# Optimization experiments

Measured on AMD Instinct MI355X. Metric: run time of the kernel, lower is better.

## Reference

```python
import jax, jax.numpy as jnp
import numpy as np

N = 10000       # nodes
E = 200000      # node pairs (edges) in rel_dict
R = 400000      # relation instances
F_IN = 128
F_OUT = 64


def setup_inputs() -> dict:
    key = jax.random.key(0)
    ks = jax.random.split(key, 8)
    x = jax.random.normal(ks[0], (N, F_IN), dtype=jnp.float32)
    rel = jax.random.normal(ks[1], (R, F_IN), dtype=jnp.float32)
    adj = jax.random.uniform(ks[2], (N, N), dtype=jnp.float32)
    edge_pairs = jax.random.randint(ks[3], (E, 2), 0, N, dtype=jnp.int32)
    rel_seg = jax.random.randint(ks[4], (R,), 0, E, dtype=jnp.int32)
    # Conv1d(in, out, kernel_size=1, bias=False) == Linear: weight [out, in]
    W = jax.random.normal(ks[5], (F_OUT, F_IN), dtype=jnp.float32) * 0.1
    w_rel = jax.random.normal(ks[6], (F_IN,), dtype=jnp.float32) * 0.1
    bias = jnp.zeros((F_OUT,), dtype=jnp.float32)
    return {"x": x, "rel": rel, "adj": adj, "edge_pairs": edge_pairs,
            "rel_seg": rel_seg, "W": W, "w_rel": w_rel, "bias": bias}


def reference(x, rel, adj, edge_pairs, rel_seg, W, w_rel, bias):
    # node transform: [N, F_OUT]
    seq_fts = x @ W.T
    # per-relation scalar: [R]
    fts_rel = rel @ w_rel
    # segment-mean per edge (vectorized form of the rel_dict loop)
    sums = jax.ops.segment_sum(fts_rel, rel_seg, num_segments=E)
    cnts = jax.ops.segment_sum(jnp.ones_like(fts_rel), rel_seg, num_segments=E)
    edge_means = sums / jnp.maximum(cnts, 1.0)  # [E]
    # symmetric scatter into dense logits [N, N]
    e1, e2 = edge_pairs[:, 0], edge_pairs[:, 1]
    logits = jnp.zeros_like(adj)
    logits = logits.at[e1, e2].set(edge_means).at[e2, e1].set(edge_means)
    # masked-ish softmax over rows, then sparse-weighted aggregation
    coefs = jax.nn.softmax(jax.nn.sigmoid(logits) + adj, axis=1)  # [N, N]
    # dropout is a no-op in eval mode (training=False)
    ret = coefs @ seq_fts + bias  # [N, F_OUT]
    return jax.nn.elu(ret)        # concat=True
```

## Files before the change

### kernel.cpp

```cpp
#include <hip/hip_runtime.h>
#include <math.h>

#define NN   10000
#define EE   200000
#define RR   400000
#define FIN  128
#define FOUT 64

#define HASH_BITS 20
#define HSIZE (1u << HASH_BITS)
#define HMASK (HSIZE - 1u)
#define ROWCAP 256

#define NKB 314

typedef __bf16 bf16x8 __attribute__((ext_vector_type(8)));
typedef __bf16 bf16x4 __attribute__((ext_vector_type(4)));
typedef float  f32x4  __attribute__((ext_vector_type(4)));

#define O_SUMS   0
#define O_CNTS   (O_SUMS + EE)
#define O_ROWCNT (O_CNTS + EE)
#define O_HKEY   (O_ROWCNT + NN)
#define O_HPRIO  (O_HKEY + HSIZE)
#define O_SEQTP  (O_HPRIO + HSIZE)
#define SEQTP_WORDS (NKB * 5 * 512 / 2)
#define ZERO_WORDS (O_SEQTP + SEQTP_WORDS)
#define O_NUMP   ZERO_WORDS
#define O_SP     (O_NUMP + 8 * NN * FOUT)
#define O_PAIRS  (O_SP + 8 * NN)

__global__ __launch_bounds__(256) void k_zero(f32x4* __restrict__ p, int n4) {
    int gid = blockIdx.x * 256 + threadIdx.x;
    if (gid < n4) p[gid] = (f32x4){0.f, 0.f, 0.f, 0.f};
}

__global__ __launch_bounds__(256) void k_seqfts(const float* __restrict__ x,
                                                const float* __restrict__ W,
                                                __bf16* __restrict__ seqTp) {
    __shared__ float Wt[FIN][FOUT + 1];
    __shared__ float xs[FIN][16 + 1];
    int t = threadIdx.x;
    for (int e = t; e < FOUT * FIN; e += 256) {
        int c = e >> 7, k = e & 127;
        Wt[k][c] = W[e];
    }
    int row0 = blockIdx.x * 16;
    for (int e = t; e < 16 * FIN; e += 256) {
        int r = e >> 7, k = e & 127;
        int gr = row0 + r;
        xs[k][r] = (gr < NN) ? x[(size_t)gr * FIN + k] : 0.f;
    }
    __syncthreads();
    int col = t & 63;
    int rg  = t >> 6;
    float acc[4] = {0.f, 0.f, 0.f, 0.f};
    for (int k = 0; k < FIN; ++k) {
        float w = Wt[k][col];
        #pragma unroll
        for (int i = 0; i < 4; ++i) acc[i] += w * xs[k][rg * 4 + i];
    }
    #pragma unroll
    for (int i = 0; i < 4; ++i) {
        int gr = row0 + rg * 4 + i;
        int kb = gr >> 5, g = (gr >> 3) & 3, slot = gr & 7;
        seqTp[((size_t)kb * 5 + (col >> 4)) * 512 + ((col & 15) + g * 16) * 8 + slot]
            = (__bf16)acc[i];
        if (col < 16)
            seqTp[((size_t)kb * 5 + 4) * 512 + (col + g * 16) * 8 + slot] = (__bf16)1.0f;
    }
}

__device__ __forceinline__ unsigned hash_cell(unsigned cell) {
    return (cell * 2654435761u) >> (32 - HASH_BITS);
}
__device__ __forceinline__ void entry_ij(const int* ep, int e, int& i, int& j, int& k) {
    k = (e < EE) ? e : e - EE;
    int a = ep[2 * k], b = ep[2 * k + 1];
    if (e < EE) { i = a; j = b; } else { i = b; j = a; }
}

#define BM 64
#define BK 64
#define KSPLIT 8
#define NCHUNK 157
#define CPK 20
#define MAINB (NCHUNK * KSPLIT)
#define ILV   11
#define MRB   (ILV * MAINB)
#define SCATAB ((2 * EE + 255) / 256)
#define GRID_MR (MRB + SCATAB)
#define LDAP 72

__global__ __launch_bounds__(256) void k_mainrel(const float* __restrict__ adj,
                                                 const __bf16* __restrict__ seqTp,
                                                 const float* __restrict__ rel,
                                                 const float* __restrict__ wrel,
                                                 const int* __restrict__ rseg,
                                                 const int* __restrict__ ep,
                                                 float* __restrict__ sums,
                                                 float* __restrict__ cnts,
                                                 unsigned* __restrict__ hkey,
                                                 unsigned* __restrict__ hprio,
                                                 float* __restrict__ Nump,
                                                 float* __restrict__ Sp) {
    __shared__ __bf16 As[2][BM][LDAP];
    int t   = threadIdx.x;
    int bid = blockIdx.x;

    if (bid >= MRB) {
        int e = (bid - MRB) * 256 + t;
        if (e >= 2 * EE) return;
        int i, j, k;
        entry_ij(ep, e, i, j, k);
        unsigned cell = (unsigned)i * NN + (unsigned)j;
        unsigned keyv = cell + 1u;
        unsigned h = hash_cell(cell);
        while (true) {
            unsigned old = atomicCAS(&hkey[h], 0u, keyv);
            if (old == 0u || old == keyv) break;
            h = (h + 1u) & HMASK;
        }
        atomicMax(&hprio[h], (unsigned)(e + 1));
        return;
    }

    if (bid % ILV) {
        int relb = bid - bid / ILV - 1;
        int lane = t & 31;
        f32x4 w = *(const f32x4*)(wrel + lane * 4);
        #pragma unroll
        for (int it = 0; it < 4; ++it) {
            int row = relb * 32 + it * 8 + (t >> 5);
            if (row < RR) {
                f32x4 v = *(const f32x4*)(rel + (size_t)row * FIN + lane * 4);
                float s = v.x * w.x + v.y * w.y + v.z * w.z + v.w * w.w;
                #pragma unroll
                for (int off = 16; off >= 1; off >>= 1) s += __shfl_xor(s, off, 64);
                if (lane == 0) {
                    int seg = rseg[row];
                    atomicAdd(&sums[seg], s);
                    atomicAdd(&cnts[seg], 1.0f);
                }
            }
        }
        return;
    }

    int mi   = bid / ILV;
    int rowc = mi % NCHUNK;
    int ks   = mi / NCHUNK;
    int row0 = rowc * BM;
    int c0   = ks * CPK;
    int c1   = min(NCHUNK, c0 + CPK);
    int w  = t >> 6, l = t & 63;
    int lr = l & 15, lk = l >> 4;
    int sr = t >> 4;
    int sk = (t & 15) * 4;

    f32x4 acc[5];
    #pragma unroll
    for (int n = 0; n < 5; ++n) acc[n] = (f32x4){0.f, 0.f, 0.f, 0.f};

    f32x4 pvA[4], pvB[4];

#define LOADA(PV, CH)                                                          \
    {                                                                          \
        int k0_ = (CH) * BK;                                                   \
        _Pragma("unroll")                                                      \
        for (int e2 = 0; e2 < 4; ++e2) {                                       \
            int gr = row0 + sr + e2 * 16;                                      \
            int gk = k0_ + sk;                                                 \
            PV[e2] = (gr < NN && gk < NN)                                      \
                         ? *(const f32x4*)(adj + (size_t)gr * NN + gk)         \
                         : (f32x4){-1e9f, -1e9f, -1e9f, -1e9f};                \
        }                                                                      \
    }

#define BODY(PV, CH, P_)                                                       \
    {                                                                          \
        _Pragma("unroll")                                                      \
        for (int e2 = 0; e2 < 4; ++e2) {                                       \
            f32x4 v = PV[e2];                                                  \
            float e0 = exp2f(fmaf(v.x, 1.442695041f, 0.7213475204f));          \
            float e1 = exp2f(fmaf(v.y, 1.442695041f, 0.7213475204f));          \
            float e2f = exp2f(fmaf(v.z, 1.442695041f, 0.7213475204f));         \
            float e3 = exp2f(fmaf(v.w, 1.442695041f, 0.7213475204f));          \
            bf16x4 q = { (__bf16)e0, (__bf16)e1, (__bf16)e2f, (__bf16)e3 };    \
            *(bf16x4*)&As[P_][sr + e2 * 16][sk] = q;                           \
        }                                                                      \
        const __bf16* bp = seqTp + (size_t)(CH) * 2 * 5 * 512 + l * 8;         \
        bf16x8 b0 = *(const bf16x8*)(bp);                                      \
        bf16x8 b1 = *(const bf16x8*)(bp + 512);                                \
        bf16x8 b2 = *(const bf16x8*)(bp + 1024);                               \
        bf16x8 b3 = *(const bf16x8*)(bp + 1536);                               \
        bf16x8 b4 = *(const bf16x8*)(bp + 2048);                               \
        __syncthreads();                                                       \
        bf16x8 a0 = *(const bf16x8*)&As[P_][w * 16 + lr][lk * 8];              \
        acc[0] = __builtin_amdgcn_mfma_f32_16x16x32_bf16(a0, b0, acc[0], 0, 0, 0); \
        acc[1] = __builtin_amdgcn_mfma_f32_16x16x32_bf16(a0, b1, acc[1], 0, 0, 0); \
        acc[2] = __builtin_amdgcn_mfma_f32_16x16x32_bf16(a0, b2, acc[2], 0, 0, 0); \
        acc[3] = __builtin_amdgcn_mfma_f32_16x16x32_bf16(a0, b3, acc[3], 0, 0, 0); \
        acc[4] = __builtin_amdgcn_mfma_f32_16x16x32_bf16(a0, b4, acc[4], 0, 0, 0); \
        const __bf16* bq = bp + 2560;                                          \
        bf16x8 d0 = *(const bf16x8*)(bq);                                      \
        bf16x8 d1 = *(const bf16x8*)(bq + 512);                                \
        bf16x8 d2 = *(const bf16x8*)(bq + 1024);                               \
        bf16x8 d3 = *(const bf16x8*)(bq + 1536);                               \
        bf16x8 d4 = *(const bf16x8*)(bq + 2048);                               \
        bf16x8 a1 = *(const bf16x8*)&As[P_][w * 16 + lr][32 + lk * 8];         \
        acc[0] = __builtin_amdgcn_mfma_f32_16x16x32_bf16(a1, d0, acc[0], 0, 0, 0); \
        acc[1] = __builtin_amdgcn_mfma_f32_16x16x32_bf16(a1, d1, acc[1], 0, 0, 0); \
        acc[2] = __builtin_amdgcn_mfma_f32_16x16x32_bf16(a1, d2, acc[2], 0, 0, 0); \
        acc[3] = __builtin_amdgcn_mfma_f32_16x16x32_bf16(a1, d3, acc[3], 0, 0, 0); \
        acc[4] = __builtin_amdgcn_mfma_f32_16x16x32_bf16(a1, d4, acc[4], 0, 0, 0); \
    }

    LOADA(pvA, c0);
    int ch = c0, p = 0;
    while (true) {
        if (ch + 1 < c1) LOADA(pvB, ch + 1);
        BODY(pvA, ch, p);
        p ^= 1; ++ch;
        if (ch >= c1) break;
        if (ch + 1 < c1) LOADA(pvA, ch + 1);
        BODY(pvB, ch, p);
        p ^= 1; ++ch;
        if (ch >= c1) break;
    }
#undef LOADA
#undef BODY

    float* nout = Nump + (size_t)ks * NN * FOUT;
    #pragma unroll
    for (int n = 0; n < 4; ++n) {
        #pragma unroll
        for (int r = 0; r < 4; ++r) {
            int grow = row0 + w * 16 + lk * 4 + r;
            if (grow < NN)
                nout[(size_t)grow * FOUT + n * 16 + lr] = acc[n][r];
        }
    }
    if (lr == 0) {
        #pragma unroll
        for (int r = 0; r < 4; ++r) {
            int grow = row0 + w * 16 + lk * 4 + r;
            if (grow < NN) Sp[(size_t)ks * NN + grow] = acc[4][r];
        }
    }
}

__global__ __launch_bounds__(256) void k_scatB(const int* __restrict__ ep,
                                               const float* __restrict__ sums,
                                               const float* __restrict__ cnts,
                                               const unsigned* __restrict__ hkey,
                                               const unsigned* __restrict__ hprio,
                                               const float* __restrict__ adj,
                                               int* __restrict__ rowcnt,
                                               uint2* __restrict__ pairs) {
    int e = blockIdx.x * 256 + threadIdx.x;
    if (e >= 2 * EE) return;
    int i, j, k;
    entry_ij(ep, e, i, j, k);
    unsigned cell = (unsigned)i * NN + (unsigned)j;
    unsigned keyv = cell + 1u;
    unsigned h = hash_cell(cell);
    while (hkey[h] != keyv) h = (h + 1u) & HMASK;
    if (hprio[h] == (unsigned)(e + 1)) {
        float v   = sums[k] / fmaxf(cnts[k], 1.0f);
        float sg  = 1.f / (1.f + __expf(-v));
        float aij = adj[(size_t)i * NN + j];
        float dw  = __expf(aij + sg) - __expf(aij + 0.5f);
        if (dw != 0.f) {
            int pos = atomicAdd(&rowcnt[i], 1);
            if (pos < ROWCAP)
                pairs[(size_t)i * ROWCAP + pos] =
                    make_uint2((unsigned)j, __float_as_uint(dw));
        }
    }
}

__global__ __launch_bounds__(256) void k_rowupd(const float* __restrict__ Nump,
                                                const float* __restrict__ Sp,
                                                const int* __restrict__ rowcnt,
                                                const uint2* __restrict__ pairs,
                                                const __bf16* __restrict__ seqTp,
                                                const float* __restrict__ bias,
                                                float* __restrict__ out) {
    int t = threadIdx.x;
    int i = blockIdx.x * 4 + (t >> 6);
    if (i >= NN) return;
    int c = t & 63;
    float acc = 0.f, sb = 0.f;
    #pragma unroll
    for (int ks = 0; ks < 8; ++ks) {
        acc += Nump[(size_t)ks * NN * FOUT + (size_t)i * FOUT + c];
        sb  += Sp[(size_t)ks * NN + i];
    }
    int cnt = min(rowcnt[i], ROWCAP);
    float sdw = 0.f;
    const uint2* pr = pairs + (size_t)i * ROWCAP;
    for (int e = 0; e < cnt; ++e) {
        uint2 pk = pr[e];
        float d  = __uint_as_float(pk.y);
        unsigned j = pk.x;
        float sj = (float)seqTp[((size_t)(j >> 5) * 5 + (c >> 4)) * 512
                                + ((c & 15) + ((j >> 3) & 3) * 16) * 8 + (j & 7)];
        acc += d * sj;
        sdw += d;
    }
    float v = acc / (sb + sdw) + bias[c];
    out[(size_t)i * FOUT + c] = (v > 0.f) ? v : expm1f(v);
}

extern "C" void kernel_launch(void* const* d_in, const int* in_sizes, int n_in,
                              void* d_out, int out_size, void* d_ws, size_t ws_size,
                              hipStream_t stream) {
    const float* x    = (const float*)d_in[0];
    const float* rel  = (const float*)d_in[1];
    const float* adj  = (const float*)d_in[2];
    const int*   ep   = (const int*)d_in[3];
    const int*   rseg = (const int*)d_in[4];
    const float* W    = (const float*)d_in[5];
    const float* wrel = (const float*)d_in[6];
    const float* bias = (const float*)d_in[7];
    float* out = (float*)d_out;

    float* ws = (float*)d_ws;
    float*    sums   = ws + O_SUMS;
    float*    cnts   = ws + O_CNTS;
    int*      rowcnt = (int*)(ws + O_ROWCNT);
    unsigned* hkey   = (unsigned*)(ws + O_HKEY);
    unsigned* hprio  = (unsigned*)(ws + O_HPRIO);
    __bf16*   seqTp  = (__bf16*)(ws + O_SEQTP);
    float*    Nump   = ws + O_NUMP;
    float*    Sp     = ws + O_SP;
    uint2*    pairs  = (uint2*)(ws + O_PAIRS);

    int n4 = ZERO_WORDS / 4;
    k_zero<<<(n4 + 255) / 256, 256, 0, stream>>>((f32x4*)d_ws, n4);
    k_seqfts<<<NN / 16, 256, 0, stream>>>(x, W, seqTp);
    k_mainrel<<<GRID_MR, 256, 0, stream>>>(adj, seqTp, rel, wrel, rseg, ep,
                                           sums, cnts, hkey, hprio, Nump, Sp);
    k_scatB<<<(2 * EE + 255) / 256, 256, 0, stream>>>(ep, sums, cnts, hkey, hprio,
                                                      adj, rowcnt, pairs);
    k_rowupd<<<(NN + 3) / 4, 256, 0, stream>>>(Nump, Sp, rowcnt, pairs,
                                               seqTp, bias, out);
}
```

Before: 319.7 us.

## Precompute bf16 exp(adj) in a conversion pass and fuse scatter into GEMM

Adds a pass that reads adj once, writes exp(adj+0.5) as a padded bf16 matrix and accumulates row sums via atomics, alongside the relation reductions and hash insertion. The GEMM kernel then streams the bf16 matrix directly, dropping the ones-column MFMA for row sums, and the edge scatter kernel is interleaved into the same launch. This removes exp work and fp32 loads from the GEMM inner loop at the cost of an extra 200MB write and read of workspace.

```diff
diff --git a/kernel.cpp b/kernel.cpp
--- a/kernel.cpp
+++ b/kernel.cpp
@@ -6,6 +6,7 @@
 #define RR   400000
 #define FIN  128
 #define FOUT 64
+#define AJP  10048
 
 #define HASH_BITS 20
 #define HSIZE (1u << HASH_BITS)
@@ -13,6 +14,8 @@
 #define ROWCAP 256
 
 #define NKB 314
+#define L2E 1.442695041f
+#define CHALF 0.7213475204f
 
 typedef __bf16 bf16x8 __attribute__((ext_vector_type(8)));
 typedef __bf16 bf16x4 __attribute__((ext_vector_type(4)));
@@ -20,15 +23,16 @@
 
 #define O_SUMS   0
 #define O_CNTS   (O_SUMS + EE)
-#define O_ROWCNT (O_CNTS + EE)
+#define O_S      (O_CNTS + EE)
+#define O_ROWCNT (O_S + NN)
 #define O_HKEY   (O_ROWCNT + NN)
 #define O_HPRIO  (O_HKEY + HSIZE)
 #define O_SEQTP  (O_HPRIO + HSIZE)
 #define SEQTP_WORDS (NKB * 5 * 512 / 2)
 #define ZERO_WORDS (O_SEQTP + SEQTP_WORDS)
-#define O_NUMP   ZERO_WORDS
-#define O_SP     (O_NUMP + 8 * NN * FOUT)
-#define O_PAIRS  (O_SP + 8 * NN)
+#define O_ADJE   ZERO_WORDS
+#define O_NUMP   (O_ADJE + NN * AJP / 2)
+#define O_PAIRS  (O_NUMP + 8 * NN * FOUT)
 
 __global__ __launch_bounds__(256) void k_zero(f32x4* __restrict__ p, int n4) {
     int gid = blockIdx.x * 256 + threadIdx.x;
@@ -66,8 +70,6 @@
         int kb = gr >> 5, g = (gr >> 3) & 3, slot = gr & 7;
         seqTp[((size_t)kb * 5 + (col >> 4)) * 512 + ((col & 15) + g * 16) * 8 + slot]
             = (__bf16)acc[i];
-        if (col < 16)
-            seqTp[((size_t)kb * 5 + 4) * 512 + (col + g * 16) * 8 + slot] = (__bf16)1.0f;
     }
 }
 
@@ -80,36 +82,25 @@
     if (e < EE) { i = a; j = b; } else { i = b; j = a; }
 }
 
-#define BM 64
-#define BK 64
-#define KSPLIT 8
-#define NCHUNK 157
-#define CPK 20
-#define MAINB (NCHUNK * KSPLIT)
-#define ILV   11
-#define MRB   (ILV * MAINB)
-#define SCATAB ((2 * EE + 255) / 256)
-#define GRID_MR (MRB + SCATAB)
-#define LDAP 72
-
-__global__ __launch_bounds__(256) void k_mainrel(const float* __restrict__ adj,
-                                                 const __bf16* __restrict__ seqTp,
+#define CRB 16250
+#define HASHB2 1563
+#define GRID_CR (CRB + HASHB2)
+
+__global__ __launch_bounds__(256) void k_convrel(const float* __restrict__ adj,
                                                  const float* __restrict__ rel,
                                                  const float* __restrict__ wrel,
                                                  const int* __restrict__ rseg,
                                                  const int* __restrict__ ep,
+                                                 __bf16* __restrict__ adjE,
+                                                 float* __restrict__ S,
                                                  float* __restrict__ sums,
                                                  float* __restrict__ cnts,
                                                  unsigned* __restrict__ hkey,
-                                                 unsigned* __restrict__ hprio,
-                                                 float* __restrict__ Nump,
-                                                 float* __restrict__ Sp) {
-    __shared__ __bf16 As[2][BM][LDAP];
-    int t   = threadIdx.x;
-    int bid = blockIdx.x;
-
-    if (bid >= MRB) {
-        int e = (bid - MRB) * 256 + t;
+                                                 unsigned* __restrict__ hprio) {
+    int t = threadIdx.x, bid = blockIdx.x;
+
+    if (bid >= CRB) {
+        int e = (bid - CRB) * 256 + t;
         if (e >= 2 * EE) return;
         int i, j, k;
         entry_ij(ep, e, i, j, k);
@@ -125,95 +116,168 @@
         return;
     }
 
-    if (bid % ILV) {
-        int relb = bid - bid / ILV - 1;
-        int lane = t & 31;
-        f32x4 w = *(const f32x4*)(wrel + lane * 4);
+    int m = bid % 13;
+    int grp = bid / 13;
+    int l = t & 63;
+
+    if (m >= 8) {
+        int relb = grp * 5 + (m - 8);
+        int lane = l & 31;
+        f32x4 wv = *(const f32x4*)(wrel + lane * 4);
+        int rbase = relb * 64 + (t >> 5);
+        f32x4 pv[8];
         #pragma unroll
-        for (int it = 0; it < 4; ++it) {
-            int row = relb * 32 + it * 8 + (t >> 5);
-            if (row < RR) {
-                f32x4 v = *(const f32x4*)(rel + (size_t)row * FIN + lane * 4);
-                float s = v.x * w.x + v.y * w.y + v.z * w.z + v.w * w.w;
-                #pragma unroll
-                for (int off = 16; off >= 1; off >>= 1) s += __shfl_xor(s, off, 64);
-                if (lane == 0) {
-                    int seg = rseg[row];
-                    atomicAdd(&sums[seg], s);
-                    atomicAdd(&cnts[seg], 1.0f);
-                }
+        for (int pass = 0; pass < 8; ++pass)
+            pv[pass] = *(const f32x4*)(rel + (size_t)(rbase + pass * 8) * FIN + lane * 4);
+        #pragma unroll
+        for (int pass = 0; pass < 8; ++pass) {
+            f32x4 v = pv[pass];
+            float s = v.x * wv.x + v.y * wv.y + v.z * wv.z + v.w * wv.w;
+            s += __shfl_xor(s, 1, 64);
+            s += __shfl_xor(s, 2, 64);
+            s += __shfl_xor(s, 4, 64);
+            s += __shfl_xor(s, 8, 64);
+            s += __shfl_xor(s, 16, 64);
+            if (lane == 0) {
+                int row = rbase + pass * 8;
+                int seg = rseg[row];
+                atomicAdd(&sums[seg], s);
+                atomicAdd(&cnts[seg], 1.0f);
             }
         }
         return;
     }
 
-    int mi   = bid / ILV;
-    int rowc = mi % NCHUNK;
-    int ks   = mi / NCHUNK;
-    int row0 = rowc * BM;
-    int c0   = ks * CPK;
-    int c1   = min(NCHUNK, c0 + CPK);
-    int w  = t >> 6, l = t & 63;
+    int row = grp * 8 + m;
+    int w = t >> 6;
+    const float* ap = adj + (size_t)row * NN + w * 2500;
+    __bf16* op = adjE + (size_t)row * AJP + w * 2500;
+
+    f32x4 pv[10];
+    #pragma unroll
+    for (int i = 0; i < 10; ++i) {
+        int off = i * 256 + l * 4;
+        pv[i] = (off < 2500) ? *(const f32x4*)(ap + off) : (f32x4){0.f, 0.f, 0.f, 0.f};
+    }
+    float psum = 0.f;
+    #pragma unroll
+    for (int i = 0; i < 10; ++i) {
+        int off = i * 256 + l * 4;
+        if (off < 2500) {
+            f32x4 v = pv[i];
+            float e0 = exp2f(fmaf(v.x, L2E, CHALF));
+            float e1 = exp2f(fmaf(v.y, L2E, CHALF));
+            float e2 = exp2f(fmaf(v.z, L2E, CHALF));
+            float e3 = exp2f(fmaf(v.w, L2E, CHALF));
+            psum += (e0 + e1) + (e2 + e3);
+            bf16x4 q = { (__bf16)e0, (__bf16)e1, (__bf16)e2, (__bf16)e3 };
+            *(bf16x4*)(op + off) = q;
+        } else if (w == 3 && (7500 + off) < AJP) {
+            bf16x4 z = { (__bf16)0.f, (__bf16)0.f, (__bf16)0.f, (__bf16)0.f };
+            *(bf16x4*)(op + off) = z;
+        }
+    }
+    psum += __shfl_xor(psum, 1, 64);
+    psum += __shfl_xor(psum, 2, 64);
+    psum += __shfl_xor(psum, 4, 64);
+    psum += __shfl_xor(psum, 8, 64);
+    psum += __shfl_xor(psum, 16, 64);
+    psum += __shfl_xor(psum, 32, 64);
+    if (l == 0) atomicAdd(&S[row], psum);
+}
+
+#define MAINB2 1256
+#define SCATB2 1563
+#define GRID_MS (2512 + (SCATB2 - 1256))
+
+__global__ __launch_bounds__(256) void k_mainscat(const __bf16* __restrict__ adjE,
+                                                  const __bf16* __restrict__ seqTp,
+                                                  const int* __restrict__ ep,
+                                                  const float* __restrict__ sums,
+                                                  const float* __restrict__ cnts,
+                                                  const unsigned* __restrict__ hkey,
+                                                  const unsigned* __restrict__ hprio,
+                                                  const float* __restrict__ adj,
+                                                  int* __restrict__ rowcnt,
+                                                  uint2* __restrict__ pairs,
+                                                  float* __restrict__ Nump) {
+    __shared__ __bf16 As[2][64][72];
+    int t = threadIdx.x, bid = blockIdx.x;
+
+    if (bid >= 2512 || (bid & 1)) {
+        int sid = (bid < 2512) ? (bid >> 1) : (1256 + bid - 2512);
+        int e = sid * 256 + t;
+        if (e >= 2 * EE) return;
+        int i, j, k;
+        entry_ij(ep, e, i, j, k);
+        unsigned cell = (unsigned)i * NN + (unsigned)j;
+        unsigned keyv = cell + 1u;
+        unsigned h = hash_cell(cell);
+        while (hkey[h] != keyv) h = (h + 1u) & HMASK;
+        if (hprio[h] == (unsigned)(e + 1)) {
+            float v   = sums[k] / fmaxf(cnts[k], 1.0f);
+            float sg  = 1.f / (1.f + __expf(-v));
+            float aij = adj[(size_t)i * NN + j];
+            float dw  = __expf(aij + sg) - __expf(aij + 0.5f);
+            if (dw != 0.f) {
+                int pos = atomicAdd(&rowcnt[i], 1);
+                if (pos < ROWCAP)
+                    pairs[(size_t)i * ROWCAP + pos] =
+                        make_uint2((unsigned)j, __float_as_uint(dw));
+            }
+        }
+        return;
+    }
+
+    int mi   = bid >> 1;
+    int rowc = mi % 157;
+    int ks   = mi / 157;
+    int row0 = rowc * 64;
+    int c0 = ks * 20, c1 = min(157, c0 + 20);
+    int w = t >> 6, l = t & 63;
     int lr = l & 15, lk = l >> 4;
-    int sr = t >> 4;
-    int sk = (t & 15) * 4;
-
-    f32x4 acc[5];
-    #pragma unroll
-    for (int n = 0; n < 5; ++n) acc[n] = (f32x4){0.f, 0.f, 0.f, 0.f};
-
-    f32x4 pvA[4], pvB[4];
+    int sr2 = t >> 3;
+    int sc8 = (t & 7) * 8;
+
+    f32x4 acc[4];
+    #pragma unroll
+    for (int n = 0; n < 4; ++n) acc[n] = (f32x4){0.f, 0.f, 0.f, 0.f};
+
+    bf16x8 pvA[2], pvB[2];
+    const bf16x8 zf = {};
 
 #define LOADA(PV, CH)                                                          \
     {                                                                          \
-        int k0_ = (CH) * BK;                                                   \
-        _Pragma("unroll")                                                      \
-        for (int e2 = 0; e2 < 4; ++e2) {                                       \
-            int gr = row0 + sr + e2 * 16;                                      \
-            int gk = k0_ + sk;                                                 \
-            PV[e2] = (gr < NN && gk < NN)                                      \
-                         ? *(const f32x4*)(adj + (size_t)gr * NN + gk)         \
-                         : (f32x4){-1e9f, -1e9f, -1e9f, -1e9f};                \
-        }                                                                      \
+        int k0_ = (CH) * 64;                                                   \
+        int r1 = row0 + sr2, r2 = row0 + 32 + sr2;                             \
+        PV[0] = (r1 < NN) ? *(const bf16x8*)(adjE + (size_t)r1 * AJP + k0_ + sc8) : zf; \
+        PV[1] = (r2 < NN) ? *(const bf16x8*)(adjE + (size_t)r2 * AJP + k0_ + sc8) : zf; \
     }
 
 #define BODY(PV, CH, P_)                                                       \
     {                                                                          \
-        _Pragma("unroll")                                                      \
-        for (int e2 = 0; e2 < 4; ++e2) {                                       \
-            f32x4 v = PV[e2];                                                  \
-            float e0 = exp2f(fmaf(v.x, 1.442695041f, 0.7213475204f));          \
-            float e1 = exp2f(fmaf(v.y, 1.442695041f, 0.7213475204f));          \
-            float e2f = exp2f(fmaf(v.z, 1.442695041f, 0.7213475204f));         \
-            float e3 = exp2f(fmaf(v.w, 1.442695041f, 0.7213475204f));          \
-            bf16x4 q = { (__bf16)e0, (__bf16)e1, (__bf16)e2f, (__bf16)e3 };    \
-            *(bf16x4*)&As[P_][sr + e2 * 16][sk] = q;                           \
-        }                                                                      \
+        *(bf16x8*)&As[P_][sr2][sc8]      = PV[0];                              \
+        *(bf16x8*)&As[P_][32 + sr2][sc8] = PV[1];                              \
         const __bf16* bp = seqTp + (size_t)(CH) * 2 * 5 * 512 + l * 8;         \
         bf16x8 b0 = *(const bf16x8*)(bp);                                      \
         bf16x8 b1 = *(const bf16x8*)(bp + 512);                                \
         bf16x8 b2 = *(const bf16x8*)(bp + 1024);                               \
         bf16x8 b3 = *(const bf16x8*)(bp + 1536);                               \
-        bf16x8 b4 = *(const bf16x8*)(bp + 2048);                               \
+        bf16x8 d0 = *(const bf16x8*)(bp + 2560);                               \
+        bf16x8 d1 = *(const bf16x8*)(bp + 3072);                               \
+        bf16x8 d2 = *(const bf16x8*)(bp + 3584);                               \
+        bf16x8 d3 = *(const bf16x8*)(bp + 4096);                               \
         __syncthreads();                                                       \
         bf16x8 a0 = *(const bf16x8*)&As[P_][w * 16 + lr][lk * 8];              \
         acc[0] = __builtin_amdgcn_mfma_f32_16x16x32_bf16(a0, b0, acc[0], 0, 0, 0); \
         acc[1] = __builtin_amdgcn_mfma_f32_16x16x32_bf16(a0, b1, acc[1], 0, 0, 0); \
         acc[2] = __builtin_amdgcn_mfma_f32_16x16x32_bf16(a0, b2, acc[2], 0, 0, 0); \
         acc[3] = __builtin_amdgcn_mfma_f32_16x16x32_bf16(a0, b3, acc[3], 0, 0, 0); \
-        acc[4] = __builtin_amdgcn_mfma_f32_16x16x32_bf16(a0, b4, acc[4], 0, 0, 0); \
-        const __bf16* bq = bp + 2560;                                          \
-        bf16x8 d0 = *(const bf16x8*)(bq);                                      \
-        bf16x8 d1 = *(const bf16x8*)(bq + 512);                                \
-        bf16x8 d2 = *(const bf16x8*)(bq + 1024);                               \
-        bf16x8 d3 = *(const bf16x8*)(bq + 1536);                               \
-        bf16x8 d4 = *(const bf16x8*)(bq + 2048);                               \
         bf16x8 a1 = *(const bf16x8*)&As[P_][w * 16 + lr][32 + lk * 8];         \
         acc[0] = __builtin_amdgcn_mfma_f32_16x16x32_bf16(a1, d0, acc[0], 0, 0, 0); \
         acc[1] = __builtin_amdgcn_mfma_f32_16x16x32_bf16(a1, d1, acc[1], 0, 0, 0); \
         acc[2] = __builtin_amdgcn_mfma_f32_16x16x32_bf16(a1, d2, acc[2], 0, 0, 0); \
         acc[3] = __builtin_amdgcn_mfma_f32_16x16x32_bf16(a1, d3, acc[3], 0, 0, 0); \
-        acc[4] = __builtin_amdgcn_mfma_f32_16x16x32_bf16(a1, d4, acc[4], 0, 0, 0); \
     }
 
     LOADA(pvA, c0);
@@ -241,47 +305,10 @@
                 nout[(size_t)grow * FOUT + n * 16 + lr] = acc[n][r];
         }
     }
-    if (lr == 0) {
-        #pragma unroll
-        for (int r = 0; r < 4; ++r) {
-            int grow = row0 + w * 16 + lk * 4 + r;
-            if (grow < NN) Sp[(size_t)ks * NN + grow] = acc[4][r];
-        }
-    }
-}
-
-__global__ __launch_bounds__(256) void k_scatB(const int* __restrict__ ep,
-                                               const float* __restrict__ sums,
-                                               const float* __restrict__ cnts,
-                                               const unsigned* __restrict__ hkey,
-                                               const unsigned* __restrict__ hprio,
-                                               const float* __restrict__ adj,
-                                               int* __restrict__ rowcnt,
-                                               uint2* __restrict__ pairs) {
-    int e = blockIdx.x * 256 + threadIdx.x;
-    if (e >= 2 * EE) return;
-    int i, j, k;
-    entry_ij(ep, e, i, j, k);
-    unsigned cell = (unsigned)i * NN + (unsigned)j;
-    unsigned keyv = cell + 1u;
-    unsigned h = hash_cell(cell);
-    while (hkey[h] != keyv) h = (h + 1u) & HMASK;
-    if (hprio[h] == (unsigned)(e + 1)) {
-        float v   = sums[k] / fmaxf(cnts[k], 1.0f);
-        float sg  = 1.f / (1.f + __expf(-v));
-        float aij = adj[(size_t)i * NN + j];
-        float dw  = __expf(aij + sg) - __expf(aij + 0.5f);
-        if (dw != 0.f) {
-            int pos = atomicAdd(&rowcnt[i], 1);
-            if (pos < ROWCAP)
-                pairs[(size_t)i * ROWCAP + pos] =
-                    make_uint2((unsigned)j, __float_as_uint(dw));
-        }
-    }
 }
 
 __global__ __launch_bounds__(256) void k_rowupd(const float* __restrict__ Nump,
-                                                const float* __restrict__ Sp,
+                                                const float* __restrict__ S,
                                                 const int* __restrict__ rowcnt,
                                                 const uint2* __restrict__ pairs,
                                                 const __bf16* __restrict__ seqTp,
@@ -291,12 +318,11 @@
     int i = blockIdx.x * 4 + (t >> 6);
     if (i >= NN) return;
     int c = t & 63;
-    float acc = 0.f, sb = 0.f;
-    #pragma unroll
-    for (int ks = 0; ks < 8; ++ks) {
+    float acc = 0.f;
+    #pragma unroll
+    for (int ks = 0; ks < 8; ++ks)
         acc += Nump[(size_t)ks * NN * FOUT + (size_t)i * FOUT + c];
-        sb  += Sp[(size_t)ks * NN + i];
-    }
+    float sb = S[i];
     int cnt = min(rowcnt[i], ROWCAP);
     float sdw = 0.f;
     const uint2* pr = pairs + (size_t)i * ROWCAP;
@@ -329,21 +355,22 @@
     float* ws = (float*)d_ws;
     float*    sums   = ws + O_SUMS;
     float*    cnts   = ws + O_CNTS;
+    float*    S      = ws + O_S;
     int*      rowcnt = (int*)(ws + O_ROWCNT);
     unsigned* hkey   = (unsigned*)(ws + O_HKEY);
     unsigned* hprio  = (unsigned*)(ws + O_HPRIO);
     __bf16*   seqTp  = (__bf16*)(ws + O_SEQTP);
+    __bf16*   adjE   = (__bf16*)(ws + O_ADJE);
     float*    Nump   = ws + O_NUMP;
-    float*    Sp     = ws + O_SP;
     uint2*    pairs  = (uint2*)(ws + O_PAIRS);
 
     int n4 = ZERO_WORDS / 4;
     k_zero<<<(n4 + 255) / 256, 256, 0, stream>>>((f32x4*)d_ws, n4);
     k_seqfts<<<NN / 16, 256, 0, stream>>>(x, W, seqTp);
-    k_mainrel<<<GRID_MR, 256, 0, stream>>>(adj, seqTp, rel, wrel, rseg, ep,
-                                           sums, cnts, hkey, hprio, Nump, Sp);
-    k_scatB<<<(2 * EE + 255) / 256, 256, 0, stream>>>(ep, sums, cnts, hkey, hprio,
-                                                      adj, rowcnt, pairs);
-    k_rowupd<<<(NN + 3) / 4, 256, 0, stream>>>(Nump, Sp, rowcnt, pairs,
+    k_convrel<<<GRID_CR, 256, 0, stream>>>(adj, rel, wrel, rseg, ep,
+                                           adjE, S, sums, cnts, hkey, hprio);
+    k_mainscat<<<GRID_MS, 256, 0, stream>>>(adjE, seqTp, ep, sums, cnts,
+                                            hkey, hprio, adj, rowcnt, pairs, Nump);
+    k_rowupd<<<(NN + 3) / 4, 256, 0, stream>>>(Nump, S, rowcnt, pairs,
                                                seqTp, bias, out);
 }
```

Measured after the change: 368.6 us. 15.3% more time.
